# Kernel optimization log

Hardware: AMD Instinct MI355X
Metric: run time of the kernel (lower is better)

## Reference

```python
import jax, jax.numpy as jnp
import numpy as np

D_MODEL = 1024
NUM_HEADS = 16
HEAD_DIM = D_MODEL // NUM_HEADS
B, L = 2, 2048


def setup_inputs() -> dict:
    key = jax.random.key(0)
    ks = jax.random.split(key, 9)
    s = 0.02
    return {
        "query": jax.random.normal(ks[0], (B, L, D_MODEL), dtype=jnp.float32),
        "key": jax.random.normal(ks[1], (B, L, D_MODEL), dtype=jnp.float32),
        "value": jax.random.normal(ks[2], (B, L, D_MODEL), dtype=jnp.float32),
        "mask": jax.random.randint(ks[3], (B, L), 0, 2, dtype=jnp.int32),
        "Wq": jax.random.normal(ks[4], (D_MODEL, D_MODEL), dtype=jnp.float32) * s,
        "Wk": jax.random.normal(ks[5], (D_MODEL, D_MODEL), dtype=jnp.float32) * s,
        "Wv": jax.random.normal(ks[6], (D_MODEL, D_MODEL), dtype=jnp.float32) * s,
        "Wo": jax.random.normal(ks[7], (D_MODEL, D_MODEL), dtype=jnp.float32) * s,
        "bo": jnp.zeros((D_MODEL,), dtype=jnp.float32),
    }


def _split_heads(x):
    # (B, L, d_model) -> (B, H, L, head_dim)
    b, l, _ = x.shape
    return x.reshape(b, l, NUM_HEADS, HEAD_DIM).transpose(0, 2, 1, 3)


def reference(query, key, value, mask, Wq, Wk, Wv, Wo, bo):
    # nn.Linear(bias=False): x @ W.T
    q = _split_heads(query @ Wq.T)   # (B, H, L, hd)
    k = _split_heads(key @ Wk.T)
    v = _split_heads(value @ Wv.T)

    scores = jnp.einsum("bhqd,bhkd->bhqk", q, k) / jnp.sqrt(jnp.float32(HEAD_DIM))
    # padding mask over keys: (B, L) -> (B, 1, 1, L); 0 = pad -> -inf
    keep = (mask[:, None, None, :] != 0)
    scores = jnp.where(keep, scores, -jnp.inf)

    attn = jax.nn.softmax(scores, axis=-1)
    # original zeroes NaN rows (fully-masked query rows)
    attn = jnp.where(jnp.isnan(attn), jnp.zeros_like(attn), attn)
    # dropout is identity in eval/reference mode

    ctx = jnp.einsum("bhqk,bhkd->bhqd", attn, v)           # (B, H, L, hd)
    ctx = ctx.transpose(0, 2, 1, 3).reshape(B, L, D_MODEL)  # combine heads
    return ctx @ Wo.T + bo
```

## Files before the change

### kernel.cpp

```cpp
#include <hip/hip_runtime.h>

typedef unsigned short u16;
typedef __bf16 bf16x8 __attribute__((ext_vector_type(8)));
typedef __bf16 bf16x4 __attribute__((ext_vector_type(4)));
typedef float floatx4 __attribute__((ext_vector_type(4)));
typedef u16 u16x4 __attribute__((ext_vector_type(4)));

#define MEG ((size_t)(1u << 20))

__device__ __forceinline__ u16 f2bf(float f) {
  unsigned int u = __float_as_uint(f);
  u += 0x7fffu + ((u >> 16) & 1u);
  return (u16)(u >> 16);
}

__device__ __forceinline__ void load_lds16(const u16* g, u16* l) {
  __builtin_amdgcn_global_load_lds((const __attribute__((address_space(1))) unsigned int*)g,
                                   (__attribute__((address_space(3))) unsigned int*)l,
                                   16, 0, 0);
}

__global__ __launch_bounds__(256) void cvt7(
    const float* __restrict__ s0, const float* __restrict__ s1,
    const float* __restrict__ s2, const float* __restrict__ s3,
    const float* __restrict__ s4, const float* __restrict__ s5,
    const float* __restrict__ s6, u16* __restrict__ dst)
{
  size_t e = ((size_t)blockIdx.x * 256 + threadIdx.x) * 4;
  unsigned m = (unsigned)(e >> 20);
  const float* s; size_t off;
  if (m < 4)       { s = s0; off = e; }
  else if (m < 8)  { s = s1; off = e - 4 * MEG; }
  else if (m < 12) { s = s2; off = e - 8 * MEG; }
  else if (m < 13) { s = s3; off = e - 12 * MEG; }
  else if (m < 14) { s = s4; off = e - 13 * MEG; }
  else if (m < 15) { s = s5; off = e - 14 * MEG; }
  else             { s = s6; off = e - 15 * MEG; }
  float4 f = *reinterpret_cast<const float4*>(s + off);
  u16x4 o;
  o.x = f2bf(f.x); o.y = f2bf(f.y); o.z = f2bf(f.z); o.w = f2bf(f.w);
  *reinterpret_cast<u16x4*>(dst + e) = o;
}

template<int IT, bool OUT_BF16, bool ADD_BIAS, bool VT>
__global__ __launch_bounds__(256) void gemm_bt(
    const u16* __restrict__ Abase, const u16* __restrict__ Bbase,
    const float* __restrict__ bias, void* __restrict__ Cbase,
    u16* __restrict__ VtB,
    int M, int N, int K, long zA, long zB, long zC)
{
  __shared__ __align__(16) u16 As[IT * 32 * 64];
  __shared__ __align__(16) u16 Bs[128 * 64];
  const int tid = threadIdx.x;
  const int w = tid >> 6, ln = tid & 63;
  const int lm = ln & 15, lq = ln >> 4;
  const int wm = w >> 1, wn = w & 1;
  const long m0 = (long)blockIdx.y * (IT * 32), n0 = (long)blockIdx.x * 128;
  const u16* A = Abase + (size_t)blockIdx.z * (size_t)zA;
  const u16* B = Bbase + (size_t)blockIdx.z * (size_t)zB;

  const int r0 = tid >> 3;
  const int kc = (tid & 7) ^ (r0 & 7);
  const u16* gA = A + (m0 + r0) * (long)K + kc * 8;
  const u16* gB = B + (n0 + r0) * (long)K + kc * 8;
  const long rstep = 32L * K;

  const int sl0 = (lq ^ (lm & 7)) * 8;
  const int sl1 = ((4 + lq) ^ (lm & 7)) * 8;
  const u16* ab0 = &As[(wm * (IT * 16) + lm) * 64 + sl0];
  const u16* ab1 = &As[(wm * (IT * 16) + lm) * 64 + sl1];
  const u16* bb0 = &Bs[(wn * 64 + lm) * 64 + sl0];
  const u16* bb1 = &Bs[(wn * 64 + lm) * 64 + sl1];

  const floatx4 z4 = {0.f, 0.f, 0.f, 0.f};
  floatx4 acc[IT][4];
#pragma unroll
  for (int i = 0; i < IT; ++i)
#pragma unroll
    for (int j = 0; j < 4; ++j) acc[i][j] = z4;

  for (int k0 = 0; k0 < K; k0 += 64) {
#pragma unroll
    for (int t = 0; t < IT; ++t)
      load_lds16(gA + t * rstep, &As[(t * 256 + w * 64) * 8]);
#pragma unroll
    for (int t = 0; t < 4; ++t)
      load_lds16(gB + t * rstep, &Bs[(t * 256 + w * 64) * 8]);
    gA += 64; gB += 64;
    __syncthreads();
    bf16x8 af[IT][2], bfr[4][2];
#pragma unroll
    for (int i = 0; i < IT; ++i) {
      af[i][0] = *reinterpret_cast<const bf16x8*>(ab0 + i * 1024);
      af[i][1] = *reinterpret_cast<const bf16x8*>(ab1 + i * 1024);
    }
#pragma unroll
    for (int j = 0; j < 4; ++j) {
      bfr[j][0] = *reinterpret_cast<const bf16x8*>(bb0 + j * 1024);
      bfr[j][1] = *reinterpret_cast<const bf16x8*>(bb1 + j * 1024);
    }
#pragma unroll
    for (int i = 0; i < IT; ++i)
#pragma unroll
      for (int j = 0; j < 4; ++j) {
        acc[i][j] = __builtin_amdgcn_mfma_f32_16x16x32_bf16(af[i][0], bfr[j][0], acc[i][j], 0, 0, 0);
        acc[i][j] = __builtin_amdgcn_mfma_f32_16x16x32_bf16(af[i][1], bfr[j][1], acc[i][j], 0, 0, 0);
      }
    __syncthreads();
  }

  if (VT && blockIdx.z == 2) {
#pragma unroll
    for (int i = 0; i < IT; ++i) {
      long row = m0 + wm * (IT * 16) + i * 16 + lq * 4;
      int bq = (int)(row >> 11);
      int l  = (int)(row & 2047);
#pragma unroll
      for (int j = 0; j < 4; ++j) {
        long col = n0 + wn * 64 + j * 16 + lm;
        int hh = (int)(col >> 6), dd = (int)(col & 63);
        u16x4 o;
        o.x = f2bf(acc[i][j][0]); o.y = f2bf(acc[i][j][1]);
        o.z = f2bf(acc[i][j][2]); o.w = f2bf(acc[i][j][3]);
        *reinterpret_cast<u16x4*>(&VtB[((size_t)(bq * 16 + hh)) * 131072 +
                                       (size_t)dd * 2048 + l]) = o;
      }
    }
    return;
  }

#pragma unroll
  for (int i = 0; i < IT; ++i) {
    long row = m0 + wm * (IT * 16) + i * 16 + lq * 4;
#pragma unroll
    for (int j = 0; j < 4; ++j) {
      long col = n0 + wn * 64 + j * 16 + lm;
#pragma unroll
      for (int r = 0; r < 4; ++r) {
        float v = acc[i][j][r];
        if (ADD_BIAS) v += bias[col];
        size_t idx = (size_t)(row + r) * (size_t)N + (size_t)col;
        if (OUT_BF16) (((u16*)Cbase) + (size_t)blockIdx.z * (size_t)zC)[idx] = f2bf(v);
        else ((float*)Cbase)[idx] = v;
      }
    }
  }
}

__global__ __launch_bounds__(256, 4) void attn_kernel(
    const u16* __restrict__ Qp, const u16* __restrict__ Kp,
    const u16* __restrict__ Vt, const int* __restrict__ mask,
    u16* __restrict__ OpBase, float* __restrict__ psAB)
{
  __shared__ __align__(16) u16 Ks[64 * 64];
  __shared__ __align__(16) u16 Vts[64 * 64];
  __shared__ __align__(16) u16 Ps[4 * 32 * 64];
  __shared__ __align__(16) u16 mball[1024];

  const int tid = threadIdx.x;
  const int w = tid >> 6, ln = tid & 63;
  const int lm = ln & 15, lq = ln >> 4;
  const int bh = blockIdx.y, b = bh >> 4, h = bh & 15;
  const int q0 = blockIdx.x * 128;
  const int kz = blockIdx.z;

  const u16* Qh = Qp + (size_t)b * 2048 * 1024 + h * 64;
  const u16* Kh = Kp + (size_t)b * 2048 * 1024 + (size_t)kz * 1024 * 1024 + h * 64;
  const u16* Vth = Vt + (size_t)bh * 64 * 2048 + kz * 1024;
  u16* Op = OpBase + (size_t)kz * 8 * MEG;
  float* psZ = psAB + (size_t)kz * 65536;

  const int* mrowp = mask + b * 2048 + kz * 1024;
#pragma unroll
  for (int t = 0; t < 4; ++t) {
    int i = t * 256 + tid;
    mball[i] = (mrowp[i] != 0) ? (u16)0 : (u16)0xFF80;
  }

  bf16x8 qf[2][2];
#pragma unroll
  for (int m = 0; m < 2; ++m) {
    int qrow = q0 + w * 32 + m * 16 + lm;
    qf[m][0] = *reinterpret_cast<const bf16x8*>(Qh + (size_t)qrow * 1024 + lq * 8);
    qf[m][1] = *reinterpret_cast<const bf16x8*>(Qh + (size_t)qrow * 1024 + 32 + lq * 8);
  }

  const int sl0 = (lq ^ (lm & 7)) * 8;
  const int sl1 = ((4 + lq) ^ (lm & 7)) * 8;
  const u16* kb0 = &Ks[lm * 64 + sl0];
  const u16* kb1 = &Ks[lm * 64 + sl1];
  const u16* vb0 = &Vts[lm * 64 + sl0];
  const u16* vb1 = &Vts[lm * 64 + sl1];
  u16* Pw = &Ps[w * 2048];
  u16* pwr[4];
#pragma unroll
  for (int n = 0; n < 4; ++n) pwr[n] = &Pw[lm * 64 + (((4 * n + lq) ^ lm) * 4)];
  const u16* prd[4];
#pragma unroll
  for (int t = 0; t < 4; ++t)
    prd[t] = &Pw[lm * 64 + (((8 * (t >> 1) + 2 * lq + (t & 1)) ^ lm) * 4)];
  const u16* mbi = mball + lq * 4;

  const int r0 = tid >> 3;
  const int kc = (tid & 7) ^ (r0 & 7);
  const u16* gK0 = Kh + (size_t)r0 * 1024 + kc * 8;
  const u16* gK1 = gK0 + 32 * 1024;
  const u16* gV0 = Vth + (size_t)r0 * 2048 + kc * 8;
  const u16* gV1 = gV0 + 32 * 2048;

  const floatx4 z4 = {0.f, 0.f, 0.f, 0.f};
  floatx4 O[2][4];
#pragma unroll
  for (int m = 0; m < 2; ++m)
#pragma unroll
    for (int j = 0; j < 4; ++j) O[m][j] = z4;
  float psum[2] = {0.f, 0.f};
  const float SCL = 0.18033688011112042f;

  for (int it = 0; it < 16; ++it) {
    load_lds16(gK0, &Ks[(w * 64) * 8]);
    load_lds16(gK1, &Ks[(256 + w * 64) * 8]);
    load_lds16(gV0, &Vts[(w * 64) * 8]);
    load_lds16(gV1, &Vts[(256 + w * 64) * 8]);
    gK0 += 64 * 1024; gK1 += 64 * 1024; gV0 += 64; gV1 += 64;
    __syncthreads();

    bf16x8 kf[4][2], vf[4][2];
#pragma unroll
    for (int n = 0; n < 4; ++n) {
      kf[n][0] = *reinterpret_cast<const bf16x8*>(kb0 + n * 1024);
      kf[n][1] = *reinterpret_cast<const bf16x8*>(kb1 + n * 1024);
    }
#pragma unroll
    for (int j = 0; j < 4; ++j) {
      vf[j][0] = *reinterpret_cast<const bf16x8*>(vb0 + j * 1024);
      vf[j][1] = *reinterpret_cast<const bf16x8*>(vb1 + j * 1024);
    }
    float mb4[4][4];
#pragma unroll
    for (int n = 0; n < 4; ++n) {
      u16x4 mv = *reinterpret_cast<const u16x4*>(mbi + n * 16);
      mb4[n][0] = __uint_as_float((unsigned)mv.x << 16);
      mb4[n][1] = __uint_as_float((unsigned)mv.y << 16);
      mb4[n][2] = __uint_as_float((unsigned)mv.z << 16);
      mb4[n][3] = __uint_as_float((unsigned)mv.w << 16);
    }
    mbi += 64;

#pragma unroll
    for (int m = 0; m < 2; ++m) {
      floatx4 S[4];
#pragma unroll
      for (int n = 0; n < 4; ++n) {
        S[n] = __builtin_amdgcn_mfma_f32_16x16x32_bf16(kf[n][0], qf[m][0], z4, 0, 0, 0);
        S[n] = __builtin_amdgcn_mfma_f32_16x16x32_bf16(kf[n][1], qf[m][1], S[n], 0, 0, 0);
      }

#pragma unroll
      for (int n = 0; n < 4; ++n) {
        float p0 = __builtin_amdgcn_exp2f(fmaf(S[n][0], SCL, mb4[n][0]));
        float p1 = __builtin_amdgcn_exp2f(fmaf(S[n][1], SCL, mb4[n][1]));
        float p2 = __builtin_amdgcn_exp2f(fmaf(S[n][2], SCL, mb4[n][2]));
        float p3 = __builtin_amdgcn_exp2f(fmaf(S[n][3], SCL, mb4[n][3]));
        psum[m] += (p0 + p1) + (p2 + p3);
        unsigned u0 = __float_as_uint(p0) + 0x8000u;
        unsigned u1 = __float_as_uint(p1) + 0x8000u;
        unsigned u2 = __float_as_uint(p2) + 0x8000u;
        unsigned u3 = __float_as_uint(p3) + 0x8000u;
        uint2 pk;
        pk.x = __builtin_amdgcn_perm(u1, u0, 0x07060302u);
        pk.y = __builtin_amdgcn_perm(u3, u2, 0x07060302u);
        *reinterpret_cast<uint2*>(pwr[n] + m * 1024) = pk;
      }

#pragma unroll
      for (int h2 = 0; h2 < 2; ++h2) {
        bf16x4 pa = *reinterpret_cast<const bf16x4*>(prd[2 * h2] + m * 1024);
        bf16x4 pb = *reinterpret_cast<const bf16x4*>(prd[2 * h2 + 1] + m * 1024);
        bf16x8 pf = __builtin_shufflevector(pa, pb, 0, 1, 2, 3, 4, 5, 6, 7);
#pragma unroll
        for (int j = 0; j < 4; ++j)
          O[m][j] = __builtin_amdgcn_mfma_f32_16x16x32_bf16(pf, vf[j][h2], O[m][j], 0, 0, 0);
      }
    }
    __syncthreads();
  }

#pragma unroll
  for (int m = 0; m < 2; ++m) {
    float s = psum[m];
    s += __shfl_xor(s, 16, 64);
    s += __shfl_xor(s, 32, 64);
    int prow = q0 + w * 32 + m * 16 + lm;
    if (lq == 0) psZ[bh * 2048 + prow] = s;
#pragma unroll
    for (int r = 0; r < 4; ++r) {
      int row = q0 + w * 32 + m * 16 + lq * 4 + r;
      size_t base = ((size_t)b * 2048 + row) * 1024 + h * 64 + lm;
#pragma unroll
      for (int j = 0; j < 4; ++j)
        Op[base + j * 16] = f2bf(O[m][j][r]);
    }
  }
}

__global__ __launch_bounds__(256) void combine_norm(
    const u16* __restrict__ Oa, const u16* __restrict__ Ob,
    const float* __restrict__ psA, const float* __restrict__ psB,
    u16* __restrict__ ctx)
{
  size_t idx = ((size_t)blockIdx.x * 256 + threadIdx.x) * 8;
  int q = (int)(idx >> 10);
  int c = (int)(idx & 1023);
  int b = q >> 11, l = q & 2047, h = c >> 6;
  int ql = (b * 16 + h) * 2048 + l;
  float s = psA[ql] + psB[ql];
  float inv = (s > 0.f) ? 1.0f / s : 0.f;

  uint4 ua = *reinterpret_cast<const uint4*>(Oa + idx);
  uint4 ub = *reinterpret_cast<const uint4*>(Ob + idx);
  uint4 uo;
  const unsigned* pa = reinterpret_cast<const unsigned*>(&ua);
  const unsigned* pb = reinterpret_cast<const unsigned*>(&ub);
  unsigned* po = reinterpret_cast<unsigned*>(&uo);
#pragma unroll
  for (int i = 0; i < 4; ++i) {
    float alo = __uint_as_float(pa[i] << 16);
    float ahi = __uint_as_float(pa[i] & 0xFFFF0000u);
    float blo = __uint_as_float(pb[i] << 16);
    float bhi = __uint_as_float(pb[i] & 0xFFFF0000u);
    float olo = (alo + blo) * inv;
    float ohi = (ahi + bhi) * inv;
    po[i] = (unsigned)f2bf(olo) | ((unsigned)f2bf(ohi) << 16);
  }
  *reinterpret_cast<uint4*>(ctx + idx) = uo;
}

extern "C" void kernel_launch(void* const* d_in, const int* in_sizes, int n_in,
                              void* d_out, int out_size, void* d_ws, size_t ws_size,
                              hipStream_t stream) {
  const float* q  = (const float*)d_in[0];
  const float* k  = (const float*)d_in[1];
  const float* v  = (const float*)d_in[2];
  const int*   mk = (const int*)  d_in[3];
  const float* wq = (const float*)d_in[4];
  const float* wk = (const float*)d_in[5];
  const float* wv = (const float*)d_in[6];
  const float* wo = (const float*)d_in[7];
  const float* bo = (const float*)d_in[8];

  u16* ws16 = (u16*)d_ws;
  u16* Xq  = ws16;
  u16* Wq  = ws16 + 12 * MEG;
  u16* Wo  = ws16 + 15 * MEG;
  u16* Qp  = ws16 + 16 * MEG;
  u16* Kp  = ws16 + 20 * MEG;
  u16* Vt  = ws16 + 24 * MEG;
  u16* OpA = ws16;
  u16* OpB = ws16 + 8 * MEG;
  float* psAB = (float*)(ws16 + 12 * MEG);
  u16* ctx = ws16 + 4 * MEG;

  cvt7<<<dim3(16384), dim3(256), 0, stream>>>(q, k, v, wq, wk, wv, wo, ws16);

  gemm_bt<4, true, false, true><<<dim3(8, 32, 3), dim3(256), 0, stream>>>(
      Xq, Wq, nullptr, (void*)Qp, Vt, 4096, 1024, 1024,
      (long)(4 * MEG), (long)MEG, (long)(4 * MEG));

  attn_kernel<<<dim3(16, 32, 2), dim3(256), 0, stream>>>(Qp, Kp, Vt, mk, OpA, psAB);

  combine_norm<<<dim3(2048), dim3(256), 0, stream>>>(OpA, OpB, psAB, psAB + 65536, ctx);

  gemm_bt<2, false, true, false><<<dim3(8, 64, 1), dim3(256), 0, stream>>>(
      ctx, Wo, bo, d_out, nullptr, 4096, 1024, 1024, 0, 0, 0);
}
```

Baseline: 222.6 us.

## Widen conversion per thread, swap GEMM grid order, store mask bias as float

The fp32-to-bf16 conversion kernel now handles 16 elements per thread with four float4 loads in flight, and launches a quarter as many blocks. Both GEMMs swap the grid x/y mapping so consecutive blocks walk along M and share the same B (weight) tile, which changes L2 reuse. In the attention kernel the key-mask bias is kept in LDS as fp32, which removes the bf16 unpacking per tile but doubles the LDS footprint of that buffer. These are small unrelated tweaks that mostly target memory traffic and instruction overhead.

```diff
diff --git a/kernel.cpp b/kernel.cpp
--- a/kernel.cpp
+++ b/kernel.cpp
@@ -26,7 +26,7 @@
     const float* __restrict__ s4, const float* __restrict__ s5,
     const float* __restrict__ s6, u16* __restrict__ dst)
 {
-  size_t e = ((size_t)blockIdx.x * 256 + threadIdx.x) * 4;
+  size_t e = ((size_t)blockIdx.x * 256 + threadIdx.x) * 16;
   unsigned m = (unsigned)(e >> 20);
   const float* s; size_t off;
   if (m < 4)       { s = s0; off = e; }
@@ -36,10 +36,16 @@
   else if (m < 14) { s = s4; off = e - 13 * MEG; }
   else if (m < 15) { s = s5; off = e - 14 * MEG; }
   else             { s = s6; off = e - 15 * MEG; }
-  float4 f = *reinterpret_cast<const float4*>(s + off);
-  u16x4 o;
-  o.x = f2bf(f.x); o.y = f2bf(f.y); o.z = f2bf(f.z); o.w = f2bf(f.w);
-  *reinterpret_cast<u16x4*>(dst + e) = o;
+  float4 f[4];
+#pragma unroll
+  for (int t = 0; t < 4; ++t)
+    f[t] = *reinterpret_cast<const float4*>(s + off + t * 4);
+#pragma unroll
+  for (int t = 0; t < 4; ++t) {
+    u16x4 o;
+    o.x = f2bf(f[t].x); o.y = f2bf(f[t].y); o.z = f2bf(f[t].z); o.w = f2bf(f[t].w);
+    *reinterpret_cast<u16x4*>(dst + e + t * 4) = o;
+  }
 }
 
 template<int IT, bool OUT_BF16, bool ADD_BIAS, bool VT>
@@ -55,7 +61,7 @@
   const int w = tid >> 6, ln = tid & 63;
   const int lm = ln & 15, lq = ln >> 4;
   const int wm = w >> 1, wn = w & 1;
-  const long m0 = (long)blockIdx.y * (IT * 32), n0 = (long)blockIdx.x * 128;
+  const long m0 = (long)blockIdx.x * (IT * 32), n0 = (long)blockIdx.y * 128;
   const u16* A = Abase + (size_t)blockIdx.z * (size_t)zA;
   const u16* B = Bbase + (size_t)blockIdx.z * (size_t)zB;
 
@@ -155,7 +161,7 @@
   __shared__ __align__(16) u16 Ks[64 * 64];
   __shared__ __align__(16) u16 Vts[64 * 64];
   __shared__ __align__(16) u16 Ps[4 * 32 * 64];
-  __shared__ __align__(16) u16 mball[1024];
+  __shared__ __align__(16) float mball[1024];
 
   const int tid = threadIdx.x;
   const int w = tid >> 6, ln = tid & 63;
@@ -174,7 +180,7 @@
 #pragma unroll
   for (int t = 0; t < 4; ++t) {
     int i = t * 256 + tid;
-    mball[i] = (mrowp[i] != 0) ? (u16)0 : (u16)0xFF80;
+    mball[i] = (mrowp[i] != 0) ? 0.f : -__builtin_inff();
   }
 
   bf16x8 qf[2][2];
@@ -199,7 +205,7 @@
 #pragma unroll
   for (int t = 0; t < 4; ++t)
     prd[t] = &Pw[lm * 64 + (((8 * (t >> 1) + 2 * lq + (t & 1)) ^ lm) * 4)];
-  const u16* mbi = mball + lq * 4;
+  const float* mbi = mball + lq * 4;
 
   const int r0 = tid >> 3;
   const int kc = (tid & 7) ^ (r0 & 7);
@@ -236,15 +242,10 @@
       vf[j][0] = *reinterpret_cast<const bf16x8*>(vb0 + j * 1024);
       vf[j][1] = *reinterpret_cast<const bf16x8*>(vb1 + j * 1024);
     }
-    float mb4[4][4];
-#pragma unroll
-    for (int n = 0; n < 4; ++n) {
-      u16x4 mv = *reinterpret_cast<const u16x4*>(mbi + n * 16);
-      mb4[n][0] = __uint_as_float((unsigned)mv.x << 16);
-      mb4[n][1] = __uint_as_float((unsigned)mv.y << 16);
-      mb4[n][2] = __uint_as_float((unsigned)mv.z << 16);
-      mb4[n][3] = __uint_as_float((unsigned)mv.w << 16);
-    }
+    float4 mb4[4];
+#pragma unroll
+    for (int n = 0; n < 4; ++n)
+      mb4[n] = *reinterpret_cast<const float4*>(mbi + n * 16);
     mbi += 64;
 
 #pragma unroll
@@ -258,10 +259,10 @@
 
 #pragma unroll
       for (int n = 0; n < 4; ++n) {
-        float p0 = __builtin_amdgcn_exp2f(fmaf(S[n][0], SCL, mb4[n][0]));
-        float p1 = __builtin_amdgcn_exp2f(fmaf(S[n][1], SCL, mb4[n][1]));
-        float p2 = __builtin_amdgcn_exp2f(fmaf(S[n][2], SCL, mb4[n][2]));
-        float p3 = __builtin_amdgcn_exp2f(fmaf(S[n][3], SCL, mb4[n][3]));
+        float p0 = __builtin_amdgcn_exp2f(fmaf(S[n][0], SCL, mb4[n].x));
+        float p1 = __builtin_amdgcn_exp2f(fmaf(S[n][1], SCL, mb4[n].y));
+        float p2 = __builtin_amdgcn_exp2f(fmaf(S[n][2], SCL, mb4[n].z));
+        float p3 = __builtin_amdgcn_exp2f(fmaf(S[n][3], SCL, mb4[n].w));
         psum[m] += (p0 + p1) + (p2 + p3);
         unsigned u0 = __float_as_uint(p0) + 0x8000u;
         unsigned u1 = __float_as_uint(p1) + 0x8000u;
@@ -361,9 +362,9 @@
   float* psAB = (float*)(ws16 + 12 * MEG);
   u16* ctx = ws16 + 4 * MEG;
 
-  cvt7<<<dim3(16384), dim3(256), 0, stream>>>(q, k, v, wq, wk, wv, wo, ws16);
-
-  gemm_bt<4, true, false, true><<<dim3(8, 32, 3), dim3(256), 0, stream>>>(
+  cvt7<<<dim3(4096), dim3(256), 0, stream>>>(q, k, v, wq, wk, wv, wo, ws16);
+
+  gemm_bt<4, true, false, true><<<dim3(32, 8, 3), dim3(256), 0, stream>>>(
       Xq, Wq, nullptr, (void*)Qp, Vt, 4096, 1024, 1024,
       (long)(4 * MEG), (long)MEG, (long)(4 * MEG));
 
@@ -371,6 +372,6 @@
 
   combine_norm<<<dim3(2048), dim3(256), 0, stream>>>(OpA, OpB, psAB, psAB + 65536, ctx);
 
-  gemm_bt<2, false, true, false><<<dim3(8, 64, 1), dim3(256), 0, stream>>>(
+  gemm_bt<2, false, true, false><<<dim3(64, 8, 1), dim3(256), 0, stream>>>(
       ctx, Wo, bo, d_out, nullptr, 4096, 1024, 1024, 0, 0, 0);
 }
```

Result: no change. 218.4 us (-1.9%).
